# Optimization experiments

Hardware: AMD Instinct MI355X
Metric: run time of the kernel (lower is better)

## Reference

```python
import jax, jax.numpy as jnp
import numpy as np
from jax import lax

N, H, W, C = 64, 256, 256, 16  # NHWC input
O, K = 16, 3                   # out_channels, kern_size


def setup_inputs() -> dict:
    key = jax.random.key(0)
    k_in, k_u, k_v, k_w = jax.random.split(key, 4)
    # glorot_normal std for shape [fan_in, fan_out]-ish 2D weights: sqrt(2/(a+b))
    u = jax.random.normal(k_u, (O, K), dtype=jnp.float32) * np.sqrt(2.0 / (O + K)).astype(np.float32)
    v = jax.random.normal(k_v, (O, K), dtype=jnp.float32) * np.sqrt(2.0 / (O + K)).astype(np.float32)
    w = jax.random.normal(k_w, (O, C), dtype=jnp.float32) * np.sqrt(2.0 / (O + C)).astype(np.float32)
    b = jnp.zeros((O,), dtype=jnp.float32)
    inputs = jax.random.normal(k_in, (N, H, W, C), dtype=jnp.float32)
    return {"inputs": inputs, "u": u, "v": v, "w": w, "b": b}


def reference(inputs, u, v, w, b):
    # CP low-rank kernel construction: kern[i,j,k,l] = v[l,i] * u[l,j] * w[l,k]
    # -> HWIO kernel of shape [K, K, C, O]
    kern = jnp.einsum('lj,lk,li->ijkl', u, w, v)
    out = lax.conv_general_dilated(
        inputs, kern,
        window_strides=(1, 1),
        padding='SAME',
        dimension_numbers=('NHWC', 'HWIO', 'NHWC'),
    )
    return jax.nn.relu(out + b)
```

## Files before the change

kernel.cpp:

```cpp
#include <hip/hip_runtime.h>
#include <hip/hip_bf16.h>

#define N_ 64
#define H_ 256
#define W_ 256
#define C_ 16
#define O_ 16

#define TW 32
#define TH 8
#define HALO_W (TW + 2)
#define HALO_H (TH + 2)
#define NHALO (HALO_W * HALO_H)
#define PSTRIDE 20

__global__ __launch_bounds__(256, 5)
void sep_conv_kernel(const float* __restrict__ in,
                     const float* __restrict__ u,
                     const float* __restrict__ v,
                     const float* __restrict__ w,
                     const float* __restrict__ b,
                     float* __restrict__ out) {
    __shared__ float t_lds[NHALO * PSTRIDE];

    const int tid = threadIdx.x;
    const int x0 = blockIdx.x * TW;
    const int y0 = blockIdx.y * TH;
    const int n  = blockIdx.z;

    const float* inbase = in + (size_t)n * H_ * W_ * C_;

    const int p0 = tid;
    const int p1 = tid + 256;
    const bool has1 = (p1 < NHALO);

    const int r0 = p0 / HALO_W, c0 = p0 - r0 * HALO_W;
    const int r1 = p1 / HALO_W, c1 = p1 - r1 * HALO_W;
    const int gy0 = y0 + r0 - 1, gx0 = x0 + c0 - 1;
    const int gy1 = y0 + r1 - 1, gx1 = x0 + c1 - 1;
    const bool in0 = (unsigned)gy0 < (unsigned)H_ && (unsigned)gx0 < (unsigned)W_;
    const bool in1 = has1 && (unsigned)gy1 < (unsigned)H_ && (unsigned)gx1 < (unsigned)W_;

    float4 A[4], B[4];
    #pragma unroll
    for (int q = 0; q < 4; ++q) A[q] = make_float4(0.f, 0.f, 0.f, 0.f);
    #pragma unroll
    for (int q = 0; q < 4; ++q) B[q] = make_float4(0.f, 0.f, 0.f, 0.f);

    if (in0) {
        const float4* s4 = (const float4*)(inbase + ((size_t)gy0 * W_ + gx0) * C_);
        #pragma unroll
        for (int q = 0; q < 4; ++q) A[q] = s4[q];
    }
    if (in1) {
        const float4* s4 = (const float4*)(inbase + ((size_t)gy1 * W_ + gx1) * C_);
        #pragma unroll
        for (int q = 0; q < 4; ++q) B[q] = s4[q];
    }

    {
        const float iv0[16] = {A[0].x, A[0].y, A[0].z, A[0].w,
                               A[1].x, A[1].y, A[1].z, A[1].w,
                               A[2].x, A[2].y, A[2].z, A[2].w,
                               A[3].x, A[3].y, A[3].z, A[3].w};
        float tv[16];
        #pragma unroll
        for (int l = 0; l < 16; ++l) {
            float s = 0.f;
            #pragma unroll
            for (int k = 0; k < 16; ++k) s = fmaf(w[l * 16 + k], iv0[k], s);
            tv[l] = s;
        }
        float4* d4 = (float4*)&t_lds[p0 * PSTRIDE];
        d4[0] = make_float4(tv[0],  tv[1],  tv[2],  tv[3]);
        d4[1] = make_float4(tv[4],  tv[5],  tv[6],  tv[7]);
        d4[2] = make_float4(tv[8],  tv[9],  tv[10], tv[11]);
        d4[3] = make_float4(tv[12], tv[13], tv[14], tv[15]);
    }
    if (has1) {
        const float iv1[16] = {B[0].x, B[0].y, B[0].z, B[0].w,
                               B[1].x, B[1].y, B[1].z, B[1].w,
                               B[2].x, B[2].y, B[2].z, B[2].w,
                               B[3].x, B[3].y, B[3].z, B[3].w};
        float tv[16];
        #pragma unroll
        for (int l = 0; l < 16; ++l) {
            float s = 0.f;
            #pragma unroll
            for (int k = 0; k < 16; ++k) s = fmaf(w[l * 16 + k], iv1[k], s);
            tv[l] = s;
        }
        float4* d4 = (float4*)&t_lds[p1 * PSTRIDE];
        d4[0] = make_float4(tv[0],  tv[1],  tv[2],  tv[3]);
        d4[1] = make_float4(tv[4],  tv[5],  tv[6],  tv[7]);
        d4[2] = make_float4(tv[8],  tv[9],  tv[10], tv[11]);
        d4[3] = make_float4(tv[12], tv[13], tv[14], tv[15]);
    }
    __syncthreads();

    const int tx = tid & (TW - 1);
    const int ty = tid >> 5;

    float acc[16];
    #pragma unroll
    for (int l = 0; l < 16; ++l) acc[l] = 0.f;

    #pragma unroll
    for (int i = 0; i < 3; ++i) {
        float h[16];
        #pragma unroll
        for (int l = 0; l < 16; ++l) h[l] = 0.f;
        #pragma unroll
        for (int j = 0; j < 3; ++j) {
            const float4* tp =
                (const float4*)&t_lds[((ty + i) * HALO_W + (tx + j)) * PSTRIDE];
            const float4 a0 = tp[0];
            const float4 a1 = tp[1];
            const float4 a2 = tp[2];
            const float4 a3 = tp[3];
            const float tvv[16] = {a0.x, a0.y, a0.z, a0.w,
                                   a1.x, a1.y, a1.z, a1.w,
                                   a2.x, a2.y, a2.z, a2.w,
                                   a3.x, a3.y, a3.z, a3.w};
            #pragma unroll
            for (int l = 0; l < 16; ++l) {
                h[l] = fmaf(u[l * 3 + j], tvv[l], h[l]);
            }
        }
        #pragma unroll
        for (int l = 0; l < 16; ++l) {
            acc[l] = fmaf(v[l * 3 + i], h[l], acc[l]);
        }
    }

    float r[16];
    #pragma unroll
    for (int l = 0; l < 16; ++l) {
        float val = acc[l] + b[l];
        r[l] = val > 0.f ? val : 0.f;
    }
    float4* o4 = (float4*)(out + (((size_t)n * H_ + (y0 + ty)) * W_ + (x0 + tx)) * C_);
    o4[0] = make_float4(r[0],  r[1],  r[2],  r[3]);
    o4[1] = make_float4(r[4],  r[5],  r[6],  r[7]);
    o4[2] = make_float4(r[8],  r[9],  r[10], r[11]);
    o4[3] = make_float4(r[12], r[13], r[14], r[15]);
}

extern "C" void kernel_launch(void* const* d_in, const int* in_sizes, int n_in,
                              void* d_out, int out_size, void* d_ws, size_t ws_size,
                              hipStream_t stream) {
    const float* in = (const float*)d_in[0];
    const float* u  = (const float*)d_in[1];
    const float* v  = (const float*)d_in[2];
    const float* w  = (const float*)d_in[3];
    const float* b  = (const float*)d_in[4];
    float* out = (float*)d_out;

    dim3 grid(W_ / TW, H_ / TH, N_);
    dim3 block(256);
    sep_conv_kernel<<<grid, block, 0, stream>>>(in, u, v, w, b, out);
}
```

Before: 465.8 us.

## Use planar float4 LDS layout and raise occupancy hint

New measurement: 457.9 us. Within noise of the previous version (-1.7%).

```diff
diff --git a/kernel.cpp b/kernel.cpp
--- a/kernel.cpp
+++ b/kernel.cpp
@@ -12,16 +12,16 @@
 #define HALO_W (TW + 2)
 #define HALO_H (TH + 2)
 #define NHALO (HALO_W * HALO_H)
-#define PSTRIDE 20
 
-__global__ __launch_bounds__(256, 5)
+
+__global__ __launch_bounds__(256, 7)
 void sep_conv_kernel(const float* __restrict__ in,
                      const float* __restrict__ u,
                      const float* __restrict__ v,
                      const float* __restrict__ w,
                      const float* __restrict__ b,
                      float* __restrict__ out) {
-    __shared__ float t_lds[NHALO * PSTRIDE];
+    __shared__ float4 t_lds[4 * NHALO];
 
     const int tid = threadIdx.x;
     const int x0 = blockIdx.x * TW;
@@ -71,11 +71,10 @@
             for (int k = 0; k < 16; ++k) s = fmaf(w[l * 16 + k], iv0[k], s);
             tv[l] = s;
         }
-        float4* d4 = (float4*)&t_lds[p0 * PSTRIDE];
-        d4[0] = make_float4(tv[0],  tv[1],  tv[2],  tv[3]);
-        d4[1] = make_float4(tv[4],  tv[5],  tv[6],  tv[7]);
-        d4[2] = make_float4(tv[8],  tv[9],  tv[10], tv[11]);
-        d4[3] = make_float4(tv[12], tv[13], tv[14], tv[15]);
+        t_lds[0 * NHALO + p0] = make_float4(tv[0],  tv[1],  tv[2],  tv[3]);
+        t_lds[1 * NHALO + p0] = make_float4(tv[4],  tv[5],  tv[6],  tv[7]);
+        t_lds[2 * NHALO + p0] = make_float4(tv[8],  tv[9],  tv[10], tv[11]);
+        t_lds[3 * NHALO + p0] = make_float4(tv[12], tv[13], tv[14], tv[15]);
     }
     if (has1) {
         const float iv1[16] = {B[0].x, B[0].y, B[0].z, B[0].w,
@@ -90,11 +89,10 @@
             for (int k = 0; k < 16; ++k) s = fmaf(w[l * 16 + k], iv1[k], s);
             tv[l] = s;
         }
-        float4* d4 = (float4*)&t_lds[p1 * PSTRIDE];
-        d4[0] = make_float4(tv[0],  tv[1],  tv[2],  tv[3]);
-        d4[1] = make_float4(tv[4],  tv[5],  tv[6],  tv[7]);
-        d4[2] = make_float4(tv[8],  tv[9],  tv[10], tv[11]);
-        d4[3] = make_float4(tv[12], tv[13], tv[14], tv[15]);
+        t_lds[0 * NHALO + p1] = make_float4(tv[0],  tv[1],  tv[2],  tv[3]);
+        t_lds[1 * NHALO + p1] = make_float4(tv[4],  tv[5],  tv[6],  tv[7]);
+        t_lds[2 * NHALO + p1] = make_float4(tv[8],  tv[9],  tv[10], tv[11]);
+        t_lds[3 * NHALO + p1] = make_float4(tv[12], tv[13], tv[14], tv[15]);
     }
     __syncthreads();
 
@@ -112,12 +110,11 @@
         for (int l = 0; l < 16; ++l) h[l] = 0.f;
         #pragma unroll
         for (int j = 0; j < 3; ++j) {
-            const float4* tp =
-                (const float4*)&t_lds[((ty + i) * HALO_W + (tx + j)) * PSTRIDE];
-            const float4 a0 = tp[0];
-            const float4 a1 = tp[1];
-            const float4 a2 = tp[2];
-            const float4 a3 = tp[3];
+            const int p = (ty + i) * HALO_W + (tx + j);
+            const float4 a0 = t_lds[0 * NHALO + p];
+            const float4 a1 = t_lds[1 * NHALO + p];
+            const float4 a2 = t_lds[2 * NHALO + p];
+            const float4 a3 = t_lds[3 * NHALO + p];
             const float tvv[16] = {a0.x, a0.y, a0.z, a0.w,
                                    a1.x, a1.y, a1.z, a1.w,
                                    a2.x, a2.y, a2.z, a2.w,
```
